# Kernel tuning notes

Hardware: AMD Instinct MI355X
Metric: run time of the kernel (lower is better)

The kernel has to match this reference:

```python
import jax, jax.numpy as jnp
import numpy as np

HIDDEN = 1024

def setup_inputs() -> dict:
    key = jax.random.key(0)
    k0, k1, k2, k3 = jax.random.split(key, 4)
    inputs = jax.random.normal(k0, (4, 2048, HIDDEN), dtype=jnp.float32)
    s = 1.0 / np.sqrt(HIDDEN)
    Wq = jax.random.normal(k1, (HIDDEN, HIDDEN), dtype=jnp.float32) * s
    Wk = jax.random.normal(k2, (HIDDEN, HIDDEN), dtype=jnp.float32) * s
    Wv = jax.random.normal(k3, (HIDDEN, HIDDEN), dtype=jnp.float32) * s
    return {"inputs": inputs, "Wq": Wq, "Wk": Wk, "Wv": Wv}

def reference(inputs, Wq, Wk, Wv):
    # nn.Linear with weight W applies x @ W.T; store Wq etc. as the torch weight.
    Q = jnp.einsum('bsd,ed->bse', inputs, Wq)  # [B,S,D]
    K = jnp.einsum('bsd,ed->bse', inputs, Wk)
    V = jnp.einsum('bsd,ed->bse', inputs, Wv)
    alpha = jnp.einsum('bqd,bkd->bqk', Q, K)   # no 1/sqrt(d) scaling, per source
    alpha = jax.nn.softmax(alpha, axis=2)
    return jnp.einsum('bqk,bkd->bqd', alpha, V)
```

## Files before the change

kernel.cpp:

```cpp
#include <hip/hip_runtime.h>
#include <math.h>


typedef unsigned short u16;
typedef signed char s8;
typedef __attribute__((ext_vector_type(8))) short bf16x8;
typedef __attribute__((ext_vector_type(4))) float f32x4;
typedef __attribute__((ext_vector_type(4))) int i32x4;

__device__ __forceinline__ u16 f2bf(float x) {
  unsigned u = __float_as_uint(x);
  unsigned r = (u + 0x7fffu + ((u >> 16) & 1u)) >> 16;
  return (u16)r;
}
__device__ __forceinline__ float bf2f(u16 h) {
  return __uint_as_float((unsigned)h << 16);
}
__device__ __forceinline__ int clamp127(int q) {
  return q < -127 ? -127 : (q > 127 ? 127 : q);
}

__device__ __forceinline__ void gload_lds16(const void* g, void* l) {
  __builtin_amdgcn_global_load_lds(
      (const __attribute__((address_space(1))) unsigned int*)(g),
      (__attribute__((address_space(3))) unsigned int*)(l), 16, 0, 0);
}

template <int N>
__device__ __forceinline__ void wait_vmcnt() {
  if constexpr (N == 0) asm volatile("s_waitcnt vmcnt(0)" ::: "memory");
  else if constexpr (N == 3) asm volatile("s_waitcnt vmcnt(3)" ::: "memory");
  else if constexpr (N == 4) asm volatile("s_waitcnt vmcnt(4)" ::: "memory");
  else if constexpr (N == 6) asm volatile("s_waitcnt vmcnt(6)" ::: "memory");
}

template <bool LO>
__global__ __launch_bounds__(256) void split_f32_kernel(
    const float* __restrict__ in, u16* __restrict__ hi, u16* __restrict__ lo,
    long long n) {
  long long i = ((long long)blockIdx.x * 256 + threadIdx.x) * 4;
  const long long step = (long long)gridDim.x * 256 * 4;
  for (; i < n; i += step) {
    float4 x = *(const float4*)(in + i);
    float xs[4] = {x.x, x.y, x.z, x.w};
    u16 hv[4], lv[4];
#pragma unroll
    for (int j = 0; j < 4; j++) {
      hv[j] = f2bf(xs[j]);
      if (LO) lv[j] = f2bf(xs[j] - bf2f(hv[j]));
    }
    ushort4 h;
    h.x = hv[0]; h.y = hv[1]; h.z = hv[2]; h.w = hv[3];
    *(ushort4*)(hi + i) = h;
    if (LO) {
      ushort4 l;
      l.x = lv[0]; l.y = lv[1]; l.z = lv[2]; l.w = lv[3];
      *(ushort4*)(lo + i) = l;
    }
  }
}

__global__ __launch_bounds__(512, 2) void gemmf(
    const u16* __restrict__ Xh, const u16* __restrict__ Xl,
    const u16* __restrict__ Wh, const u16* __restrict__ Wl,
    s8* __restrict__ Ca, s8* __restrict__ Cb) {
  constexpr int PL = 8192;
  __shared__ u16 lds[2 * 4 * PL];

  const int tid = threadIdx.x;
  const int ln = tid & 63;
  const int wid = tid >> 6;
  const int wm = wid >> 2;
  const int wn = wid & 3;
  const int m0 = blockIdx.y * 256;
  const int n0 = blockIdx.x * 256;

  f32x4 acc[8][4];
  const f32x4 zero = {0.f, 0.f, 0.f, 0.f};
#pragma unroll
  for (int i = 0; i < 8; i++)
#pragma unroll
    for (int j = 0; j < 4; j++) acc[i][j] = zero;

  auto stage = [&](int t) {
    u16* slot = lds + (t & 1) * 4 * PL;
    const int k0 = t << 5;
#pragma unroll
    for (int l = 0; l < 2; ++l) {
      const int c = tid + l * 512;
      const int row = ((c >> 6) << 4) + (c & 15);
      const int kk = ((c >> 4) & 3) * 8;
      gload_lds16(Xh + (size_t)(m0 + row) * 1024 + k0 + kk, slot + c * 8);
      gload_lds16(Xl + (size_t)(m0 + row) * 1024 + k0 + kk,
                  slot + PL + c * 8);
      gload_lds16(Wh + (size_t)(n0 + row) * 1024 + k0 + kk,
                  slot + 2 * PL + c * 8);
      gload_lds16(Wl + (size_t)(n0 + row) * 1024 + k0 + kk,
                  slot + 3 * PL + c * 8);
    }
  };

  stage(0);
  wait_vmcnt<0>();
  __builtin_amdgcn_s_barrier();
  __builtin_amdgcn_sched_barrier(0);

  for (int t = 0; t < 32; ++t) {
    if (t + 1 < 32) stage(t + 1);
    const u16* Ah = lds + (t & 1) * 4 * PL;
    const u16* Al = Ah + PL;
    const u16* Bh = Ah + 2 * PL;
    const u16* Bl = Ah + 3 * PL;
    const int fo = ln * 8;
    bf16x8 bh[4], bl[4];
#pragma unroll
    for (int j = 0; j < 4; ++j) {
      bh[j] = *(const bf16x8*)(Bh + (wn * 4 + j) * 512 + fo);
      bl[j] = *(const bf16x8*)(Bl + (wn * 4 + j) * 512 + fo);
    }
    __builtin_amdgcn_s_setprio(1);
#pragma unroll
    for (int mh = 0; mh < 2; ++mh) {
      bf16x8 ah[4], al[4];
#pragma unroll
      for (int i = 0; i < 4; ++i) {
        ah[i] = *(const bf16x8*)(Ah + (wm * 8 + mh * 4 + i) * 512 + fo);
        al[i] = *(const bf16x8*)(Al + (wm * 8 + mh * 4 + i) * 512 + fo);
      }
#pragma unroll
      for (int i = 0; i < 4; ++i)
#pragma unroll
        for (int j = 0; j < 4; ++j) {
          f32x4 v = acc[mh * 4 + i][j];
          v = __builtin_amdgcn_mfma_f32_16x16x32_bf16(ah[i], bh[j], v, 0, 0, 0);
          v = __builtin_amdgcn_mfma_f32_16x16x32_bf16(ah[i], bl[j], v, 0, 0, 0);
          v = __builtin_amdgcn_mfma_f32_16x16x32_bf16(al[i], bh[j], v, 0, 0, 0);
          acc[mh * 4 + i][j] = v;
        }
    }
    __builtin_amdgcn_s_setprio(0);
    if (t + 1 < 32) {
      wait_vmcnt<0>();
      __builtin_amdgcn_s_barrier();
      __builtin_amdgcn_sched_barrier(0);
    }
  }

  const int orow = (ln >> 4) * 4;
  const int ocol = ln & 15;
#pragma unroll
  for (int mi = 0; mi < 8; ++mi)
#pragma unroll
    for (int ni = 0; ni < 4; ++ni) {
      const int rbase = m0 + wm * 128 + mi * 16 + orow;
      const int cc = n0 + wn * 64 + ni * 16 + ocol;
#pragma unroll
      for (int i = 0; i < 4; ++i) {
        const float v = acc[mi][ni][i];
        const long long off = (long long)(rbase + i) * 2048 + cc;
        const int qa = clamp127(__float2int_rn(v * 16.f));
        const int qb = clamp127(__float2int_rn((v - qa * 0.0625f) * 2048.f));
        Ca[off] = (s8)qa;
        Cb[off] = (s8)qb;
      }
    }
}

__global__ __launch_bounds__(512, 2) void g2(
    const s8* __restrict__ Aa, const s8* __restrict__ Ab,
    const s8* __restrict__ Ba, const s8* __restrict__ Bb,
    u16* __restrict__ Ch, u16* __restrict__ Cl,
    int K, int lda, int ldb, int ldc,
    long long sA, long long sB, long long sC,
    float scaleA, float scaleC) {
  constexpr int APL = 128 * 64;
  constexpr int BPL = 256 * 64;
  constexpr int SLOT = 2 * APL + 2 * BPL;
  __shared__ s8 lds[3 * SLOT];

  const int tid = threadIdx.x;
  const int ln = tid & 63;
  const int wid = tid >> 6;
  const int wm = wid >> 2;
  const int wn = wid & 3;
  const int m0 = blockIdx.y * 128;
  const int n0 = blockIdx.x * 256;
  const int z = blockIdx.z;
  const long long za = (long long)z * sA;
  const long long zb = (long long)z * sB;

  const int NT = K >> 6;

  i32x4 accA[4][4], accC[4][4];
  const i32x4 izero = {0, 0, 0, 0};
#pragma unroll
  for (int i = 0; i < 4; i++)
#pragma unroll
    for (int j = 0; j < 4; j++) { accA[i][j] = izero; accC[i][j] = izero; }

  auto stage = [&](int t) {
    s8* slot = lds + (t % 3) * SLOT;
    const int k0 = t << 6;
    const s8* pAa = Aa + za + (size_t)m0 * lda + k0;
    const s8* pAb = Ab + za + (size_t)m0 * lda + k0;
    const s8* pBa = Ba + zb + (size_t)n0 * ldb + k0;
    const s8* pBb = Bb + zb + (size_t)n0 * ldb + k0;
    {
      const int c = tid;
      const int row = ((c >> 6) << 4) + (c & 15);
      const int kk = ((c >> 4) & 3) * 16;
      gload_lds16(pAa + (size_t)row * lda + kk, slot + c * 16);
      gload_lds16(pAb + (size_t)row * lda + kk, slot + APL + c * 16);
    }
#pragma unroll
    for (int l = 0; l < 2; ++l) {
      const int c = tid + l * 512;
      const int row = ((c >> 6) << 4) + (c & 15);
      const int kk = ((c >> 4) & 3) * 16;
      gload_lds16(pBa + (size_t)row * ldb + kk, slot + 2 * APL + c * 16);
      gload_lds16(pBb + (size_t)row * ldb + kk,
                  slot + 2 * APL + BPL + c * 16);
    }
  };

  stage(0);
  stage(1);
  wait_vmcnt<6>();
  __builtin_amdgcn_s_barrier();
  __builtin_amdgcn_sched_barrier(0);

  for (int t = 0; t < NT; ++t) {
    if (t + 2 < NT) stage(t + 2);
    const s8* Sa = lds + (t % 3) * SLOT;
    const s8* Sb = Sa + APL;
    const s8* Sba = Sa + 2 * APL;
    const s8* Sbb = Sba + BPL;
    const int fo = (ln >> 4) * 256 + (ln & 15) * 16;
    i32x4 aa[4], ab[4], ba[4], bb[4];
#pragma unroll
    for (int j = 0; j < 4; ++j) {
      ba[j] = *(const i32x4*)(Sba + (wn * 4 + j) * 1024 + fo);
      bb[j] = *(const i32x4*)(Sbb + (wn * 4 + j) * 1024 + fo);
    }
#pragma unroll
    for (int i = 0; i < 4; ++i) {
      aa[i] = *(const i32x4*)(Sa + (wm * 4 + i) * 1024 + fo);
      ab[i] = *(const i32x4*)(Sb + (wm * 4 + i) * 1024 + fo);
    }
    __builtin_amdgcn_s_setprio(1);
#pragma unroll
    for (int i = 0; i < 4; ++i)
#pragma unroll
      for (int j = 0; j < 4; ++j) {
        accA[i][j] = __builtin_amdgcn_mfma_i32_16x16x64_i8(
            aa[i], ba[j], accA[i][j], 0, 0, 0);
        accC[i][j] = __builtin_amdgcn_mfma_i32_16x16x64_i8(
            aa[i], bb[j], accC[i][j], 0, 0, 0);
        accC[i][j] = __builtin_amdgcn_mfma_i32_16x16x64_i8(
            ab[i], ba[j], accC[i][j], 0, 0, 0);
      }
    __builtin_amdgcn_s_setprio(0);
    if (t + 1 < NT) {
      if (t + 2 < NT) wait_vmcnt<6>();
      else            wait_vmcnt<0>();
      __builtin_amdgcn_s_barrier();
      __builtin_amdgcn_sched_barrier(0);
    }
  }

  const int orow = (ln >> 4) * 4;
  const int ocol = ln & 15;
#pragma unroll
  for (int mi = 0; mi < 4; ++mi)
#pragma unroll
    for (int ni = 0; ni < 4; ++ni) {
      const int rbase = m0 + wm * 64 + mi * 16 + orow;
      const int cc = n0 + wn * 64 + ni * 16 + ocol;
#pragma unroll
      for (int i = 0; i < 4; ++i) {
        const float v = (float)accA[mi][ni][i] * scaleA +
                        (float)accC[mi][ni][i] * scaleC;
        const long long off =
            (long long)(rbase + i) * ldc + cc + (long long)z * sC;
        const u16 h = f2bf(v);
        Ch[off] = h;
        Cl[off] = f2bf(v - bf2f(h));
      }
    }
}

template <int NSEG, int STORE, int M_REP>
__global__ __launch_bounds__(512, 2) void gemmc(
    const u16* __restrict__ A0, const u16* __restrict__ A1,
    const u16* __restrict__ A2, const u16* __restrict__ B0,
    const u16* __restrict__ B1, const u16* __restrict__ B2,
    float* __restrict__ Cf, u16* __restrict__ Ch, u16* __restrict__ Cl,
    int Kseg, int lda, int ldb, int ldc,
    long long sA, long long sB, long long sC) {
  constexpr int BM = 32 * M_REP;
  constexpr int ASZ = BM * 32;
  constexpr int BSZ = 8192;
  constexpr int SLOT = ASZ + BSZ;
  constexpr int LA = M_REP / 4;
  constexpr int L = LA + 2;
  __shared__ u16 lds[3 * SLOT];

  const int tid = threadIdx.x;
  const int ln = tid & 63;
  const int wid = tid >> 6;
  const int wm = wid >> 2;
  const int wn = wid & 3;
  const int m0 = blockIdx.y * BM;
  const int n0 = blockIdx.x * 256;
  const int z = blockIdx.z;
  const long long za = (long long)z * sA;
  const long long zb = (long long)z * sB;

  const int NT = NSEG * (Kseg >> 5);

  f32x4 acc[M_REP][4];
  const f32x4 zero = {0.f, 0.f, 0.f, 0.f};
#pragma unroll
  for (int i = 0; i < M_REP; i++)
#pragma unroll
    for (int j = 0; j < 4; j++) acc[i][j] = zero;

  auto baseA = [&](int t) -> const u16* {
    int kk = t << 5;
    const u16* p = A0;
    if (NSEG >= 2 && kk >= Kseg) { kk -= Kseg; p = A1; }
    if (NSEG >= 3 && kk >= Kseg) { kk -= Kseg; p = A2; }
    return p + za + (size_t)m0 * lda + kk;
  };
  auto baseB = [&](int t) -> const u16* {
    int kk = t << 5;
    const u16* p = B0;
    if (NSEG >= 2 && kk >= Kseg) { kk -= Kseg; p = B1; }
    if (NSEG >= 3 && kk >= Kseg) { kk -= Kseg; p = B2; }
    return p + zb + (size_t)n0 * ldb + kk;
  };
  auto stage = [&](int t) {
    u16* slot = lds + (t % 3) * SLOT;
    const u16* Ab = baseA(t);
    const u16* Bb = baseB(t);
#pragma unroll
    for (int l = 0; l < LA; ++l) {
      const int c = tid + l * 512;
      const int row = ((c >> 6) << 4) + (c & 15);
      const int kk = ((c >> 4) & 3) * 8;
      gload_lds16(Ab + (size_t)row * lda + kk, slot + c * 8);
    }
#pragma unroll
    for (int l = 0; l < 2; ++l) {
      const int c = tid + l * 512;
      const int row = ((c >> 6) << 4) + (c & 15);
      const int kk = ((c >> 4) & 3) * 8;
      gload_lds16(Bb + (size_t)row * ldb + kk, slot + ASZ + c * 8);
    }
  };

  stage(0);
  stage(1);
  wait_vmcnt<L>();
  __builtin_amdgcn_s_barrier();
  __builtin_amdgcn_sched_barrier(0);

  for (int t = 0; t < NT; ++t) {
    if (t + 2 < NT) stage(t + 2);
    const u16* Abuf = lds + (t % 3) * SLOT;
    const u16* Bbuf = Abuf + ASZ;
    const int fo = ln * 8;
    bf16x8 a[M_REP], b[4];
#pragma unroll
    for (int j = 0; j < 4; ++j)
      b[j] = *(const bf16x8*)(Bbuf + (wn * 4 + j) * 512 + fo);
#pragma unroll
    for (int i = 0; i < M_REP; ++i)
      a[i] = *(const bf16x8*)(Abuf + (wm * M_REP + i) * 512 + fo);
    __builtin_amdgcn_s_setprio(1);
#pragma unroll
    for (int i = 0; i < M_REP; ++i)
#pragma unroll
      for (int j = 0; j < 4; ++j)
        acc[i][j] = __builtin_amdgcn_mfma_f32_16x16x32_bf16(
            a[i], b[j], acc[i][j], 0, 0, 0);
    __builtin_amdgcn_s_setprio(0);
    if (t + 1 < NT) {
      if (t + 2 < NT) wait_vmcnt<L>();
      else            wait_vmcnt<0>();
      __builtin_amdgcn_s_barrier();
      __builtin_amdgcn_sched_barrier(0);
    }
  }

  const int orow = (ln >> 4) * 4;
  const int ocol = ln & 15;
#pragma unroll
  for (int mi = 0; mi < M_REP; ++mi)
#pragma unroll
    for (int ni = 0; ni < 4; ++ni) {
      const int rbase = m0 + wm * (M_REP * 16) + mi * 16 + orow;
      const int cc = n0 + wn * 64 + ni * 16 + ocol;
#pragma unroll
      for (int i = 0; i < 4; ++i) {
        const float v = acc[mi][ni][i];
        const long long off =
            (long long)(rbase + i) * ldc + cc + (long long)z * sC;
        if (STORE == 0) {
          Cf[off] = v;
        } else if (STORE == 1) {
          const u16 h = f2bf(v);
          Ch[off] = h;
          Cl[off] = f2bf(v - bf2f(h));
        } else {
          Ch[off] = f2bf(v);
        }
      }
    }
}

__device__ __forceinline__ float blk_max(float v, float* red) {
  const int wv = threadIdx.x >> 6, lnn = threadIdx.x & 63;
#pragma unroll
  for (int off = 32; off; off >>= 1) v = fmaxf(v, __shfl_xor(v, off));
  if (lnn == 0) red[wv] = v;
  __syncthreads();
  return fmaxf(fmaxf(red[0], red[1]), fmaxf(red[2], red[3]));
}
__device__ __forceinline__ float blk_sum(float v, float* red) {
  const int wv = threadIdx.x >> 6, lnn = threadIdx.x & 63;
#pragma unroll
  for (int off = 32; off; off >>= 1) v += __shfl_xor(v, off);
  if (lnn == 0) red[wv] = v;
  __syncthreads();
  return red[0] + red[1] + red[2] + red[3];
}

__global__ __launch_bounds__(256) void softmax_inplace(float* __restrict__ L) {
  float* p = L + (size_t)blockIdx.x * 2048;
  const int t = threadIdx.x;
  __shared__ float redm[4];
  __shared__ float reds[4];
  float4 x0 = *(const float4*)(p + t * 4);
  float4 x1 = *(const float4*)(p + 1024 + t * 4);
  float m = fmaxf(fmaxf(fmaxf(x0.x, x0.y), fmaxf(x0.z, x0.w)),
                  fmaxf(fmaxf(x1.x, x1.y), fmaxf(x1.z, x1.w)));
  m = blk_max(m, redm);
  float e[8];
  e[0] = __expf(x0.x - m); e[1] = __expf(x0.y - m);
  e[2] = __expf(x0.z - m); e[3] = __expf(x0.w - m);
  e[4] = __expf(x1.x - m); e[5] = __expf(x1.y - m);
  e[6] = __expf(x1.z - m); e[7] = __expf(x1.w - m);
  float s = e[0] + e[1] + e[2] + e[3] + e[4] + e[5] + e[6] + e[7];
  s = blk_sum(s, reds);
  const float inv = 1.f / s;
  u16* q = (u16*)p;
  ushort4 o0, o1;
  o0.x = f2bf(e[0] * inv); o0.y = f2bf(e[1] * inv);
  o0.z = f2bf(e[2] * inv); o0.w = f2bf(e[3] * inv);
  o1.x = f2bf(e[4] * inv); o1.y = f2bf(e[5] * inv);
  o1.z = f2bf(e[6] * inv); o1.w = f2bf(e[7] * inv);
  *(ushort4*)(q + t * 4) = o0;
  *(ushort4*)(q + 1024 + t * 4) = o1;
}

__global__ __launch_bounds__(256) void softmax_split(
    u16* __restrict__ Lh, const u16* __restrict__ Ll) {
  u16* ph = Lh + (size_t)blockIdx.x * 2048;
  const u16* pl = Ll + (size_t)blockIdx.x * 2048;
  const int t = threadIdx.x;
  __shared__ float redm[4];
  __shared__ float reds[4];
  ushort4 h0 = *(const ushort4*)(ph + t * 4);
  ushort4 h1 = *(const ushort4*)(ph + 1024 + t * 4);
  ushort4 l0 = *(const ushort4*)(pl + t * 4);
  ushort4 l1 = *(const ushort4*)(pl + 1024 + t * 4);
  float x[8];
  x[0] = bf2f(h0.x) + bf2f(l0.x); x[1] = bf2f(h0.y) + bf2f(l0.y);
  x[2] = bf2f(h0.z) + bf2f(l0.z); x[3] = bf2f(h0.w) + bf2f(l0.w);
  x[4] = bf2f(h1.x) + bf2f(l1.x); x[5] = bf2f(h1.y) + bf2f(l1.y);
  x[6] = bf2f(h1.z) + bf2f(l1.z); x[7] = bf2f(h1.w) + bf2f(l1.w);
  float m = fmaxf(fmaxf(fmaxf(x[0], x[1]), fmaxf(x[2], x[3])),
                  fmaxf(fmaxf(x[4], x[5]), fmaxf(x[6], x[7])));
  m = blk_max(m, redm);
  float e[8];
#pragma unroll
  for (int j = 0; j < 8; ++j) e[j] = __expf(x[j] - m);
  float s = e[0] + e[1] + e[2] + e[3] + e[4] + e[5] + e[6] + e[7];
  s = blk_sum(s, reds);
  const float inv = 1.f / s;
  ushort4 o0, o1;
  o0.x = f2bf(e[0] * inv); o0.y = f2bf(e[1] * inv);
  o0.z = f2bf(e[2] * inv); o0.w = f2bf(e[3] * inv);
  o1.x = f2bf(e[4] * inv); o1.y = f2bf(e[5] * inv);
  o1.z = f2bf(e[6] * inv); o1.w = f2bf(e[7] * inv);
  *(ushort4*)(ph + t * 4) = o0;
  *(ushort4*)(ph + 1024 + t * 4) = o1;
}

extern "C" void kernel_launch(void* const* d_in, const int* in_sizes, int n_in,
                              void* d_out, int out_size, void* d_ws, size_t ws_size,
                              hipStream_t stream) {
  constexpr int Bn = 4, S = 2048, D = 1024;
  constexpr long long TOK = (long long)Bn * S;
  constexpr long long DD = (long long)D * D;
  const float* X = (const float*)d_in[0];
  const float* Wq = (const float*)d_in[1];
  const float* Wk = (const float*)d_in[2];
  const float* Wv = (const float*)d_in[3];
  float* out = (float*)d_out;
  const dim3 blk(256);
  const dim3 gblk(512);

  char* w = (char*)d_ws;
  auto au16 = [&](long long n) { u16* p = (u16*)w; w += n * 2; return p; };
  auto as8 = [&](long long n) { s8* p = (s8*)w; w += n; return p; };

  if (ws_size >= (size_t)127926272ULL) {
    u16* Xh = au16(TOK * D);
    u16* Xl = au16(TOK * D);
    u16* Wch = au16(2 * DD);
    u16* Wcl = au16(2 * DD);
    u16* Wvh = au16(DD);
    s8* QKa = as8(TOK * 2 * D);
    s8* QKb = as8(TOK * 2 * D);
    u16* VT = au16((long long)D * TOK);
    u16* Ll = au16(TOK * S);
    u16* Lh = (u16*)d_ws;

    split_f32_kernel<true><<<2048, blk, 0, stream>>>(X, Xh, Xl, TOK * D);
    split_f32_kernel<true><<<512, blk, 0, stream>>>(Wq, Wch, Wcl, DD);
    split_f32_kernel<true><<<512, blk, 0, stream>>>(Wk, Wch + DD, Wcl + DD, DD);
    split_f32_kernel<false><<<512, blk, 0, stream>>>(Wv, Wvh, nullptr, DD);

    gemmf<<<dim3(8, 32, 1), gblk, 0, stream>>>(
        Xh, Xl, Wch, Wcl, QKa, QKb);
    gemmc<1, 2, 4><<<dim3(32, 8, 1), gblk, 0, stream>>>(
        Wvh, nullptr, nullptr, Xh, nullptr, nullptr, nullptr, VT, nullptr,
        D, D, D, (int)TOK, 0, 0, 0);

    g2<<<dim3(8, 16, 4), gblk, 0, stream>>>(
        QKa, QKb, QKa + D, QKb + D, Lh, Ll,
        D, 2 * D, 2 * D, S,
        (long long)S * 2 * D, (long long)S * 2 * D, (long long)S * S,
        3.90625e-3f, 3.0517578125e-5f);
    softmax_split<<<dim3(4 * S), blk, 0, stream>>>(Lh, Ll);
    gemmc<1, 0, 4><<<dim3(4, 16, 4), gblk, 0, stream>>>(
        Lh, nullptr, nullptr, VT, nullptr, nullptr,
        out, nullptr, nullptr, S, S, (int)TOK, D,
        (long long)S * S, (long long)S, (long long)S * D);
  } else {
    u16* Xh = au16(TOK * D);
    u16* Xl = au16(TOK * D);
    u16* Wch = au16(2 * DD);
    u16* Wcl = au16(2 * DD);
    u16* Wvh = au16(DD);
    u16* QKhb = au16((long long)S * 2 * D);
    u16* QKlb = au16((long long)S * 2 * D);
    u16* VTb = au16((long long)D * S);
    float* Lb = (float*)w;

    split_f32_kernel<true><<<2048, blk, 0, stream>>>(X, Xh, Xl, TOK * D);
    split_f32_kernel<true><<<512, blk, 0, stream>>>(Wq, Wch, Wcl, DD);
    split_f32_kernel<true><<<512, blk, 0, stream>>>(Wk, Wch + DD, Wcl + DD, DD);
    split_f32_kernel<false><<<512, blk, 0, stream>>>(Wv, Wvh, nullptr, DD);

    for (int b = 0; b < Bn; ++b) {
      const long long xo = (long long)b * S * D;
      gemmc<3, 1, 8><<<dim3(8, 8, 1), gblk, 0, stream>>>(
          Xh + xo, Xh + xo, Xl + xo, Wch, Wcl, Wch, nullptr, QKhb, QKlb,
          D, D, D, 2 * D, 0, 0, 0);
      gemmc<1, 2, 4><<<dim3(8, 8, 1), gblk, 0, stream>>>(
          Wvh, nullptr, nullptr, Xh + xo, nullptr, nullptr, nullptr, VTb,
          nullptr, D, D, D, S, 0, 0, 0);
      gemmc<3, 0, 4><<<dim3(8, 16, 1), gblk, 0, stream>>>(
          QKhb, QKhb, QKlb, QKhb + D, QKlb + D, QKhb + D,
          Lb, nullptr, nullptr, D, 2 * D, 2 * D, S, 0, 0, 0);
      softmax_inplace<<<dim3(S), blk, 0, stream>>>(Lb);
      gemmc<1, 0, 4><<<dim3(4, 16, 1), gblk, 0, stream>>>(
          (const u16*)Lb, nullptr, nullptr, VTb, nullptr, nullptr,
          out + xo, nullptr, nullptr, S, 2 * S, S, D, 0, 0, 0);
    }
  }
}
```

Before: 272.3 us.

## Add K=64 triple-buffered bf16 GEMM and merge weight split launches

Adds a new single-segment bf16 GEMM kernel that stages 64-wide K tiles into a three-slot LDS ring and issues two MFMAs per tile pair, and uses it for both the V projection and the attention-times-V GEMM. This replaces the generic gemmc path, aiming to halve the barrier and wait count per K and deepen the prefetch. The three weight split launches are also merged into one launch over blockIdx.z. The larger LDS footprint may reduce occupancy.

```diff
diff --git a/kernel.cpp b/kernel.cpp
--- a/kernel.cpp
+++ b/kernel.cpp
@@ -53,6 +53,36 @@
     h.x = hv[0]; h.y = hv[1]; h.z = hv[2]; h.w = hv[3];
     *(ushort4*)(hi + i) = h;
     if (LO) {
+      ushort4 l;
+      l.x = lv[0]; l.y = lv[1]; l.z = lv[2]; l.w = lv[3];
+      *(ushort4*)(lo + i) = l;
+    }
+  }
+}
+
+__global__ __launch_bounds__(256) void quantW3_kernel(
+    const float* __restrict__ Wq, const float* __restrict__ Wk,
+    const float* __restrict__ Wv, u16* __restrict__ Wch,
+    u16* __restrict__ Wcl, u16* __restrict__ Wvh, long long n) {
+  const int z = blockIdx.z;
+  const float* src = (z == 0) ? Wq : ((z == 1) ? Wk : Wv);
+  u16* hi = (z == 0) ? Wch : ((z == 1) ? (Wch + n) : Wvh);
+  u16* lo = (z == 0) ? Wcl : ((z == 1) ? (Wcl + n) : nullptr);
+  long long i = ((long long)blockIdx.x * 256 + threadIdx.x) * 4;
+  const long long step = (long long)gridDim.x * 256 * 4;
+  for (; i < n; i += step) {
+    float4 x = *(const float4*)(src + i);
+    float xs[4] = {x.x, x.y, x.z, x.w};
+    u16 hv[4], lv[4];
+#pragma unroll
+    for (int j = 0; j < 4; j++) {
+      hv[j] = f2bf(xs[j]);
+      lv[j] = f2bf(xs[j] - bf2f(hv[j]));
+    }
+    ushort4 h;
+    h.x = hv[0]; h.y = hv[1]; h.z = hv[2]; h.w = hv[3];
+    *(ushort4*)(hi + i) = h;
+    if (z < 2) {
       ushort4 l;
       l.x = lv[0]; l.y = lv[1]; l.z = lv[2]; l.w = lv[3];
       *(ushort4*)(lo + i) = l;
@@ -285,6 +315,118 @@
         const u16 h = f2bf(v);
         Ch[off] = h;
         Cl[off] = f2bf(v - bf2f(h));
+      }
+    }
+}
+
+template <int STORE>
+__global__ __launch_bounds__(512, 2) void gemmc64(
+    const u16* __restrict__ A0, const u16* __restrict__ B0,
+    float* __restrict__ Cf, u16* __restrict__ Ch,
+    int K, int lda, int ldb, int ldc,
+    long long sA, long long sB, long long sC) {
+  constexpr int ASZ = 128 * 64;
+  constexpr int BSZ = 256 * 64;
+  constexpr int SLOT = ASZ + BSZ;
+  __shared__ u16 lds[3 * SLOT];
+
+  const int tid = threadIdx.x;
+  const int ln = tid & 63;
+  const int wid = tid >> 6;
+  const int wm = wid >> 2;
+  const int wn = wid & 3;
+  const int m0 = blockIdx.y * 128;
+  const int n0 = blockIdx.x * 256;
+  const int z = blockIdx.z;
+  const long long za = (long long)z * sA;
+  const long long zb = (long long)z * sB;
+
+  const int NT = K >> 6;
+
+  f32x4 acc[4][4];
+  const f32x4 zero = {0.f, 0.f, 0.f, 0.f};
+#pragma unroll
+  for (int i = 0; i < 4; i++)
+#pragma unroll
+    for (int j = 0; j < 4; j++) acc[i][j] = zero;
+
+  auto stage = [&](int t) {
+    u16* slot = lds + (t % 3) * SLOT;
+    const int k0 = t << 6;
+    const u16* Ab = A0 + za + (size_t)m0 * lda + k0;
+    const u16* Bb = B0 + zb + (size_t)n0 * ldb + k0;
+#pragma unroll
+    for (int l = 0; l < 2; ++l) {
+      const int c = tid + l * 512;
+      const int row = ((c >> 7) << 4) + (c & 15);
+      const int kk = ((c >> 4) & 7) * 8;
+      gload_lds16(Ab + (size_t)row * lda + kk, slot + c * 8);
+    }
+#pragma unroll
+    for (int l = 0; l < 4; ++l) {
+      const int c = tid + l * 512;
+      const int row = ((c >> 7) << 4) + (c & 15);
+      const int kk = ((c >> 4) & 7) * 8;
+      gload_lds16(Bb + (size_t)row * ldb + kk, slot + ASZ + c * 8);
+    }
+  };
+
+  stage(0);
+  stage(1);
+  wait_vmcnt<6>();
+  __builtin_amdgcn_s_barrier();
+  __builtin_amdgcn_sched_barrier(0);
+
+  for (int t = 0; t < NT; ++t) {
+    if (t + 2 < NT) stage(t + 2);
+    const u16* Abuf = lds + (t % 3) * SLOT;
+    const u16* Bbuf = Abuf + ASZ;
+    const int fo = ln * 8;
+    bf16x8 a0[4], a1[4], b0[4], b1[4];
+#pragma unroll
+    for (int j = 0; j < 4; ++j) {
+      b0[j] = *(const bf16x8*)(Bbuf + (wn * 4 + j) * 1024 + fo);
+      b1[j] = *(const bf16x8*)(Bbuf + (wn * 4 + j) * 1024 + 512 + fo);
+    }
+#pragma unroll
+    for (int i = 0; i < 4; ++i) {
+      a0[i] = *(const bf16x8*)(Abuf + (wm * 4 + i) * 1024 + fo);
+      a1[i] = *(const bf16x8*)(Abuf + (wm * 4 + i) * 1024 + 512 + fo);
+    }
+    __builtin_amdgcn_s_setprio(1);
+#pragma unroll
+    for (int i = 0; i < 4; ++i)
+#pragma unroll
+      for (int j = 0; j < 4; ++j) {
+        acc[i][j] = __builtin_amdgcn_mfma_f32_16x16x32_bf16(
+            a0[i], b0[j], acc[i][j], 0, 0, 0);
+        acc[i][j] = __builtin_amdgcn_mfma_f32_16x16x32_bf16(
+            a1[i], b1[j], acc[i][j], 0, 0, 0);
+      }
+    __builtin_amdgcn_s_setprio(0);
+    if (t + 1 < NT) {
+      if (t + 2 < NT) wait_vmcnt<6>();
+      else            wait_vmcnt<0>();
+      __builtin_amdgcn_s_barrier();
+      __builtin_amdgcn_sched_barrier(0);
+    }
+  }
+
+  const int orow = (ln >> 4) * 4;
+  const int ocol = ln & 15;
+#pragma unroll
+  for (int mi = 0; mi < 4; ++mi)
+#pragma unroll
+    for (int ni = 0; ni < 4; ++ni) {
+      const int rbase = m0 + wm * 64 + mi * 16 + orow;
+      const int cc = n0 + wn * 64 + ni * 16 + ocol;
+#pragma unroll
+      for (int i = 0; i < 4; ++i) {
+        const float v = acc[mi][ni][i];
+        const long long off =
+            (long long)(rbase + i) * ldc + cc + (long long)z * sC;
+        if (STORE == 0) Cf[off] = v;
+        else            Ch[off] = f2bf(v);
       }
     }
 }
@@ -529,15 +671,13 @@
     u16* Lh = (u16*)d_ws;
 
     split_f32_kernel<true><<<2048, blk, 0, stream>>>(X, Xh, Xl, TOK * D);
-    split_f32_kernel<true><<<512, blk, 0, stream>>>(Wq, Wch, Wcl, DD);
-    split_f32_kernel<true><<<512, blk, 0, stream>>>(Wk, Wch + DD, Wcl + DD, DD);
-    split_f32_kernel<false><<<512, blk, 0, stream>>>(Wv, Wvh, nullptr, DD);
+    quantW3_kernel<<<dim3(256, 1, 3), blk, 0, stream>>>(
+        Wq, Wk, Wv, Wch, Wcl, Wvh, DD);
 
     gemmf<<<dim3(8, 32, 1), gblk, 0, stream>>>(
         Xh, Xl, Wch, Wcl, QKa, QKb);
-    gemmc<1, 2, 4><<<dim3(32, 8, 1), gblk, 0, stream>>>(
-        Wvh, nullptr, nullptr, Xh, nullptr, nullptr, nullptr, VT, nullptr,
-        D, D, D, (int)TOK, 0, 0, 0);
+    gemmc64<2><<<dim3(32, 8, 1), gblk, 0, stream>>>(
+        Wvh, Xh, nullptr, VT, D, D, D, (int)TOK, 0, 0, 0);
 
     g2<<<dim3(8, 16, 4), gblk, 0, stream>>>(
         QKa, QKb, QKa + D, QKb + D, Lh, Ll,
@@ -545,9 +685,8 @@
         (long long)S * 2 * D, (long long)S * 2 * D, (long long)S * S,
         3.90625e-3f, 3.0517578125e-5f);
     softmax_split<<<dim3(4 * S), blk, 0, stream>>>(Lh, Ll);
-    gemmc<1, 0, 4><<<dim3(4, 16, 4), gblk, 0, stream>>>(
-        Lh, nullptr, nullptr, VT, nullptr, nullptr,
-        out, nullptr, nullptr, S, S, (int)TOK, D,
+    gemmc64<0><<<dim3(4, 16, 4), gblk, 0, stream>>>(
+        Lh, VT, out, nullptr, S, S, (int)TOK, D,
         (long long)S * S, (long long)S, (long long)S * D);
   } else {
     u16* Xh = au16(TOK * D);
```

New measurement: 266.7 us. -2.1%, faster.
